# Optimization experiments

Hardware: AMD Instinct MI355X
Metric: run time of the kernel (lower is better)

The kernel has to match this reference:

```python
import jax, jax.numpy as jnp
import numpy as np

WIDTH = 1024
HEADS = 16
INIT_SCALE = 0.02


def setup_inputs() -> dict:
    key = jax.random.key(0)
    ks = jax.random.split(key, 5)
    x = jax.random.normal(ks[0], (2, 2048, WIDTH), dtype=jnp.float32)
    # torch Linear weight [out, in]; we store transposed [in, out] for x @ W
    W_qkv = jax.random.normal(ks[1], (WIDTH, 3 * WIDTH), dtype=jnp.float32) * INIT_SCALE
    b_qkv = jnp.zeros((3 * WIDTH,), dtype=jnp.float32)
    W_proj = jax.random.normal(ks[2], (WIDTH, WIDTH), dtype=jnp.float32) * INIT_SCALE
    b_proj = jnp.zeros((WIDTH,), dtype=jnp.float32)
    return {"x": x, "W_qkv": W_qkv, "b_qkv": b_qkv, "W_proj": W_proj, "b_proj": b_proj}


def reference(x, W_qkv, b_qkv, W_proj, b_proj):
    bs, n_ctx, width = x.shape
    heads = HEADS
    attn_ch = width // heads  # per-head channel dim (width*3 // heads // 3)
    scale = 1.0 / np.sqrt(np.sqrt(attn_ch))  # applied to both q and k

    qkv = x @ W_qkv + b_qkv                      # [b, t, 3*width]
    qkv = qkv.reshape(bs, n_ctx, heads, 3 * attn_ch)
    q, k, v = jnp.split(qkv, 3, axis=-1)         # each [b, t, h, c]

    weight = jnp.einsum('bthc,bshc->bhts', q * scale, k * scale)
    wdtype = weight.dtype
    weight = jax.nn.softmax(weight.astype(jnp.float32), axis=-1).astype(wdtype)

    out = jnp.einsum('bhts,bshc->bthc', weight, v).reshape(bs, n_ctx, width)
    return out @ W_proj + b_proj
```

## Files before the change

### kernel.cpp

```cpp
#include <hip/hip_runtime.h>

typedef __attribute__((ext_vector_type(4))) float fx4;
typedef __attribute__((ext_vector_type(16))) float f32x16;
typedef __attribute__((ext_vector_type(8))) short s16x8;
typedef __attribute__((ext_vector_type(2))) unsigned int u32x2;

#define QK_SCALE 0.35355339059327373f
#define LOG2E    1.4426950408889634f

__device__ __forceinline__ short f2bf(float f) {
  union { float f; unsigned int u; } v; v.f = f;
  unsigned int r = v.u + 0x7fffu + ((v.u >> 16) & 1u);
  return (short)(r >> 16);
}

__device__ __forceinline__ unsigned f2u(float f) {
  union { float f; unsigned u; } v; v.f = f; return v.u;
}
__device__ __forceinline__ float u2f(unsigned u) {
  union { unsigned u; float f; } v; v.u = u; return v.f;
}
__device__ __forceinline__ float bf2f(short s) {
  return u2f(((unsigned)(unsigned short)s) << 16);
}

__device__ __forceinline__ float xhalf_sum(float x) {
  u32x2 r = __builtin_amdgcn_permlane32_swap(f2u(x), f2u(x), false, false);
  return u2f(r[0]) + u2f(r[1]);
}

__device__ __forceinline__ int swz(int row, int cb) {
  return (row * 128 + cb) ^ ((row & 7) << 4);
}

#define GLL(g, lds) __builtin_amdgcn_global_load_lds( \
    (__attribute__((address_space(1))) void*)(void*)(g), \
    (__attribute__((address_space(3))) void*)(void*)(lds), 16, 0, 0)

__global__ __launch_bounds__(256) void prep(
    const float* __restrict__ x, short* __restrict__ x16,
    const float* __restrict__ Wqkv, short* __restrict__ WqkvT,
    const float* __restrict__ Wproj, short* __restrict__ WprojT) {
  const int b = blockIdx.x;
  if (b < 4096) {
    int i = b * 256 + threadIdx.x;
    float4 v = reinterpret_cast<const float4*>(x)[i];
    short4 o;
    o.x = f2bf(v.x); o.y = f2bf(v.y); o.z = f2bf(v.z); o.w = f2bf(v.w);
    reinterpret_cast<short4*>(x16)[i] = o;
    return;
  }
  __shared__ float tile[32][33];
  const float* W; short* WT; int N, bx, by;
  if (b < 7168) { W = Wqkv; WT = WqkvT; N = 3072; int r = b - 4096; bx = r % 96; by = r / 96; }
  else          { W = Wproj; WT = WprojT; N = 1024; int r = b - 7168; bx = r % 32; by = r / 32; }
  const int K = 1024;
  int tx = threadIdx.x & 31, ty = threadIdx.x >> 5;
  int n0 = bx * 32, k0 = by * 32;
#pragma unroll
  for (int i = 0; i < 32; i += 8)
    tile[ty + i][tx] = W[(size_t)(k0 + ty + i) * N + n0 + tx];
  __syncthreads();
#pragma unroll
  for (int i = 0; i < 32; i += 8)
    WT[(size_t)(n0 + ty + i) * K + k0 + tx] = f2bf(tile[tx][ty + i]);
}

template <int MODE, int BK>
__global__ __launch_bounds__(256) void gemm_bf16(
    const short* __restrict__ A, const short* __restrict__ Bt,
    const float* __restrict__ bias, float* __restrict__ Cout,
    short* __restrict__ Qo, short* __restrict__ Ko, short* __restrict__ Vo,
    int M, int N, int K) {
  __shared__ __align__(16) char sA[2][128 * BK * 2];
  __shared__ __align__(16) char sB[2][128 * BK * 2];
  const int tid = threadIdx.x;
  const int w = tid >> 6, l = tid & 63;
  const int lr = l & 15, lg = l >> 4;
  const int bid = blockIdx.x;
  const int m0 = ((bid & 7) * 4 + ((bid >> 3) & 3)) * 128;
  const int n0 = (bid >> 5) * 128;
  const int wr = (w >> 1) * 64, wc = (w & 1) * 64;

  fx4 accT[4][4] = {};

  auto stage = [&](int kt, int buf) {
#pragma unroll
    for (int i = 0; i < (BK == 64 ? 4 : 2); ++i) {
      int c = i * 256 + tid;
      int r, lch;
      if (BK == 64) { r = c >> 3; int p = c & 7; lch = p ^ (r & 7); }
      else          { r = c >> 2; int p = c & 3; lch = p ^ (r & 3); }
      GLL(A + (size_t)(m0 + r) * K + kt + lch * 8, sA[buf] + c * 16);
      GLL(Bt + (size_t)(n0 + r) * K + kt + lch * 8, sB[buf] + c * 16);
    }
  };

  stage(0, 0);
  __syncthreads();

  const int NIT = K / BK;
  int cur = 0;
  for (int it = 0; it < NIT; ++it) {
    if (it + 1 < NIT) stage((it + 1) * BK, cur ^ 1);
#pragma unroll
    for (int kk = 0; kk < (BK == 64 ? 2 : 1); ++kk) {
      s16x8 av[4], bv[4];
#pragma unroll
      for (int m = 0; m < 4; ++m) {
        int R = wr + m * 16 + lr;
        int off = (BK == 64) ? swz(R, kk * 64 + lg * 16)
                             : ((R * 64 + lg * 16) ^ ((R & 3) << 4));
        av[m] = *reinterpret_cast<const s16x8*>(sA[cur] + off);
      }
#pragma unroll
      for (int n = 0; n < 4; ++n) {
        int R = wc + n * 16 + lr;
        int off = (BK == 64) ? swz(R, kk * 64 + lg * 16)
                             : ((R * 64 + lg * 16) ^ ((R & 3) << 4));
        bv[n] = *reinterpret_cast<const s16x8*>(sB[cur] + off);
      }
#pragma unroll
      for (int n = 0; n < 4; ++n)
#pragma unroll
        for (int m = 0; m < 4; ++m)
          accT[n][m] = __builtin_amdgcn_mfma_f32_16x16x32_bf16(bv[n], av[m], accT[n][m], 0, 0, 0);
    }
    __syncthreads();
    cur ^= 1;
  }

#pragma unroll
  for (int n = 0; n < 4; ++n) {
    const int col0 = n0 + wc + n * 16 + lg * 4;
    const float4 bs = *reinterpret_cast<const float4*>(bias + col0);
    if (MODE == 1) {
#pragma unroll
      for (int m = 0; m < 4; ++m) {
        int row = m0 + wr + m * 16 + lr;
        float4 v;
        v.x = accT[n][m][0] + bs.x; v.y = accT[n][m][1] + bs.y;
        v.z = accT[n][m][2] + bs.z; v.w = accT[n][m][3] + bs.w;
        *reinterpret_cast<float4*>(Cout + (size_t)row * N + col0) = v;
      }
    } else {
      const int h = col0 / 192;
      const int rr = col0 - h * 192;
#pragma unroll
      for (int m = 0; m < 4; ++m) {
        int row = m0 + wr + m * 16 + lr;
        int b = row >> 11, t = row & 2047;
        size_t bh = (size_t)b * 16 + h;
        float v0 = accT[n][m][0] + bs.x, v1 = accT[n][m][1] + bs.y;
        float v2 = accT[n][m][2] + bs.z, v3 = accT[n][m][3] + bs.w;
        if (rr < 64) {
          short4 s4;
          s4.x = f2bf(v0 * (QK_SCALE * LOG2E)); s4.y = f2bf(v1 * (QK_SCALE * LOG2E));
          s4.z = f2bf(v2 * (QK_SCALE * LOG2E)); s4.w = f2bf(v3 * (QK_SCALE * LOG2E));
          *reinterpret_cast<short4*>(Qo + (bh * 2048 + t) * 64 + rr) = s4;
        } else if (rr < 128) {
          short4 s4;
          s4.x = f2bf(v0 * QK_SCALE); s4.y = f2bf(v1 * QK_SCALE);
          s4.z = f2bf(v2 * QK_SCALE); s4.w = f2bf(v3 * QK_SCALE);
          *reinterpret_cast<short4*>(Ko + (bh * 2048 + t) * 64 + (rr - 64)) = s4;
        } else {
          Vo[(bh * 64 + (rr - 128) + 0) * 2048 + t] = f2bf(v0);
          Vo[(bh * 64 + (rr - 128) + 1) * 2048 + t] = f2bf(v1);
          Vo[(bh * 64 + (rr - 128) + 2) * 2048 + t] = f2bf(v2);
          Vo[(bh * 64 + (rr - 128) + 3) * 2048 + t] = f2bf(v3);
        }
      }
    }
  }
}

__global__ __launch_bounds__(256, 4) void attn_fwd(
    const short* __restrict__ Q, const short* __restrict__ Kc,
    const short* __restrict__ VT, short* __restrict__ OW,
    float* __restrict__ ML) {
  __shared__ __align__(16) char sK[2][8192];
  __shared__ __align__(16) char sV[2][8192];
  const int tid = threadIdx.x;
  const int w = tid >> 6, l = tid & 63;
  const int l31 = l & 31, hi = l >> 5;
  const int bid = blockIdx.x;
  const int bh = (bid & 7) * 4 + ((bid >> 3) & 3);
  const int rest = bid >> 5;
  const int qt = rest >> 1, half = rest & 1;
  const int q0 = qt * 128 + w * 32;
  const int sbase = half * 1024;

  s16x8 qf[4];
  const short* qp = Q + ((size_t)bh * 2048 + q0 + l31) * 64 + hi * 8;
#pragma unroll
  for (int ks = 0; ks < 4; ++ks)
    qf[ks] = *reinterpret_cast<const s16x8*>(qp + ks * 16);

  float lsum = 0.f;
  f32x16 o0 = {}, o1 = {};

#pragma unroll
  for (int i = 0; i < 2; ++i) {
    int c = i * 256 + tid, r = c >> 3, pch = c & 7, lch = pch ^ (r & 7);
    GLL(Kc + ((size_t)bh * 2048 + sbase + r) * 64 + lch * 8, sK[0] + c * 16);
    GLL(VT + ((size_t)bh * 64 + r) * 2048 + sbase + lch * 8, sV[0] + c * 16);
  }
  __syncthreads();

  for (int sb = 0; sb < 16; ++sb) {
    const int s0 = sbase + sb * 64;
    if (sb < 15) {
#pragma unroll
      for (int i = 0; i < 2; ++i) {
        int c = i * 256 + tid, r = c >> 3, pch = c & 7, lch = pch ^ (r & 7);
        GLL(Kc + ((size_t)bh * 2048 + s0 + 64 + r) * 64 + lch * 8, sK[(sb + 1) & 1] + c * 16);
        GLL(VT + ((size_t)bh * 64 + r) * 2048 + s0 + 64 + lch * 8, sV[(sb + 1) & 1] + c * 16);
      }
    }
    const char* kb = sK[sb & 1];
    const char* vb = sV[sb & 1];

    f32x16 p0 = {}, p1 = {};
    __builtin_amdgcn_s_setprio(1);
#pragma unroll
    for (int ks = 0; ks < 4; ++ks) {
      int off = swz(l31, ks * 32 + hi * 16);
      s16x8 ka0 = *reinterpret_cast<const s16x8*>(kb + off);
      s16x8 ka1 = *reinterpret_cast<const s16x8*>(kb + off + 4096);
      p0 = __builtin_amdgcn_mfma_f32_32x32x16_bf16(ka0, qf[ks], p0, 0, 0, 0);
      p1 = __builtin_amdgcn_mfma_f32_32x32x16_bf16(ka1, qf[ks], p1, 0, 0, 0);
    }
    __builtin_amdgcn_s_setprio(0);

#pragma unroll
    for (int i = 0; i < 16; ++i) {
      p0[i] = __builtin_amdgcn_exp2f(p0[i]);
      p1[i] = __builtin_amdgcn_exp2f(p1[i]);
    }
    float s8[8];
#pragma unroll
    for (int i = 0; i < 8; ++i)
      s8[i] = (p0[2 * i] + p0[2 * i + 1]) + (p1[2 * i] + p1[2 * i + 1]);
    float rs = ((s8[0] + s8[1]) + (s8[2] + s8[3])) + ((s8[4] + s8[5]) + (s8[6] + s8[7]));
    lsum += xhalf_sum(rs);

    int wd[16];
#pragma unroll
    for (int i = 0; i < 8; ++i) {
      asm("v_cvt_pk_bf16_f32 %0, %1, %2" : "=v"(wd[i]) : "v"(p0[2 * i]), "v"(p0[2 * i + 1]));
      asm("v_cvt_pk_bf16_f32 %0, %1, %2" : "=v"(wd[8 + i]) : "v"(p1[2 * i]), "v"(p1[2 * i + 1]));
    }

    __builtin_amdgcn_s_setprio(1);
#pragma unroll
    for (int t = 0; t < 4; ++t) {
      u32x2 s02 = __builtin_amdgcn_permlane32_swap(
          (unsigned)wd[4 * t], (unsigned)wd[4 * t + 2], false, false);
      u32x2 s13 = __builtin_amdgcn_permlane32_swap(
          (unsigned)wd[4 * t + 1], (unsigned)wd[4 * t + 3], false, false);
      union { unsigned i4[4]; s16x8 v; } fr;
      fr.i4[0] = s02[0]; fr.i4[1] = s13[0]; fr.i4[2] = s02[1]; fr.i4[3] = s13[1];
      int off = swz(l31, t * 32 + hi * 16);
      s16x8 v0 = *reinterpret_cast<const s16x8*>(vb + off);
      s16x8 v1 = *reinterpret_cast<const s16x8*>(vb + off + 4096);
      o0 = __builtin_amdgcn_mfma_f32_32x32x16_bf16(v0, fr.v, o0, 0, 0, 0);
      o1 = __builtin_amdgcn_mfma_f32_32x32x16_bf16(v1, fr.v, o1, 0, 0, 0);
    }
    __builtin_amdgcn_s_setprio(0);
    __syncthreads();
  }

  short* owp = OW + (((size_t)(half * 32 + bh) * 2048) + q0 + l31) * 64 + hi * 4;
#pragma unroll
  for (int gq = 0; gq < 4; ++gq) {
    short4 s4;
    s4.x = f2bf(o0[4 * gq]);     s4.y = f2bf(o0[4 * gq + 1]);
    s4.z = f2bf(o0[4 * gq + 2]); s4.w = f2bf(o0[4 * gq + 3]);
    *reinterpret_cast<short4*>(owp + 8 * gq) = s4;
    s4.x = f2bf(o1[4 * gq]);     s4.y = f2bf(o1[4 * gq + 1]);
    s4.z = f2bf(o1[4 * gq + 2]); s4.w = f2bf(o1[4 * gq + 3]);
    *reinterpret_cast<short4*>(owp + 32 + 8 * gq) = s4;
  }
  if (hi == 0)
    ML[(size_t)(half * 32 + bh) * 2048 + q0 + l31] = lsum;
}

__global__ __launch_bounds__(256) void attn_merge(
    const short* __restrict__ OW, const float* __restrict__ ML,
    short* __restrict__ Y) {
  int gid = blockIdx.x * 256 + threadIdx.x;
  int row = gid >> 3, dc = (gid & 7) * 8;
  float inv = 1.f / (ML[row] + ML[65536 + row]);
  s16x8 a = *reinterpret_cast<const s16x8*>(OW + (size_t)row * 64 + dc);
  s16x8 bb = *reinterpret_cast<const s16x8*>(OW + (size_t)65536 * 64 + (size_t)row * 64 + dc);
  int bh = row >> 11, q = row & 2047;
  int b = bh >> 4, h = bh & 15;
  short* yp = Y + ((size_t)b * 2048 + q) * 1024 + h * 64 + dc;
  s16x8 o;
#pragma unroll
  for (int i = 0; i < 8; ++i)
    o[i] = f2bf((bf2f(a[i]) + bf2f(bb[i])) * inv);
  *reinterpret_cast<s16x8*>(yp) = o;
}

extern "C" void kernel_launch(void* const* d_in, const int* in_sizes, int n_in,
                              void* d_out, int out_size, void* d_ws, size_t ws_size,
                              hipStream_t stream) {
  const float* x     = (const float*)d_in[0];
  const float* Wqkv  = (const float*)d_in[1];
  const float* bqkv  = (const float*)d_in[2];
  const float* Wproj = (const float*)d_in[3];
  const float* bproj = (const float*)d_in[4];
  float* out = (float*)d_out;

  char* ws = (char*)d_ws;
  const size_t MB = 1024 * 1024;
  short* x16    = (short*)(ws);
  short* WqkvT  = (short*)(ws + 8 * MB);
  short* WprojT = (short*)(ws + 14 * MB);
  short* Q16    = (short*)(ws + 16 * MB);
  short* K16    = (short*)(ws + 24 * MB);
  short* VT16   = (short*)(ws + 32 * MB);
  short* OW     = (short*)(ws + 40 * MB);
  float* ML     = (float*)(ws + 58 * MB);
  short* Y16    = x16;

  prep<<<8192, 256, 0, stream>>>(x, x16, Wqkv, WqkvT, Wproj, WprojT);
  gemm_bf16<0, 32><<<768, 256, 0, stream>>>(x16, WqkvT, bqkv, nullptr,
                                            Q16, K16, VT16, 4096, 3072, 1024);
  attn_fwd<<<1024, 256, 0, stream>>>(Q16, K16, VT16, OW, ML);
  attn_merge<<<2048, 256, 0, stream>>>(OW, ML, Y16);
  gemm_bf16<1, 64><<<256, 256, 0, stream>>>(Y16, WprojT, bproj, out,
                                            nullptr, nullptr, nullptr, 4096, 1024, 1024);
}
```

Before: 120.5 us.

## Parametrize GEMM tile width, use 8 waves for QKV and narrower proj tiles

The GEMM template gains a BN parameter, and each wave now computes a 64x32 subtile instead of 64x64. The QKV GEMM keeps its 128x128 tiles but runs 512 threads (8 waves) per block. The output projection uses 128x64 tiles, doubling its grid to 512 blocks for better CU coverage. Separately, the attention kernel moves the cross-half row-sum reduction out of the KV loop so it runs once at the end, trading less per-tile shuffle work for more blocks or waves and smaller per-wave reuse.

```diff
diff --git a/kernel.cpp b/kernel.cpp
--- a/kernel.cpp
+++ b/kernel.cpp
@@ -66,34 +66,49 @@
     WT[(size_t)(n0 + ty + i) * K + k0 + tx] = f2bf(tile[tx][ty + i]);
 }
 
-template <int MODE, int BK>
-__global__ __launch_bounds__(256) void gemm_bf16(
+template <int MODE, int BK, int BN>
+__global__ __launch_bounds__(BN * 4, 4) void gemm_bf16(
     const short* __restrict__ A, const short* __restrict__ Bt,
     const float* __restrict__ bias, float* __restrict__ Cout,
     short* __restrict__ Qo, short* __restrict__ Ko, short* __restrict__ Vo,
     int M, int N, int K) {
+  constexpr int T = BN * 4;
+  constexpr int NWC = BN / 32;
+  constexpr int CA = 16 * BK / T;
+  constexpr int CB = BK / 32;
   __shared__ __align__(16) char sA[2][128 * BK * 2];
-  __shared__ __align__(16) char sB[2][128 * BK * 2];
+  __shared__ __align__(16) char sB[2][BN * BK * 2];
   const int tid = threadIdx.x;
   const int w = tid >> 6, l = tid & 63;
   const int lr = l & 15, lg = l >> 4;
   const int bid = blockIdx.x;
   const int m0 = ((bid & 7) * 4 + ((bid >> 3) & 3)) * 128;
-  const int n0 = (bid >> 5) * 128;
-  const int wr = (w >> 1) * 64, wc = (w & 1) * 64;
-
-  fx4 accT[4][4] = {};
+  const int n0 = (bid >> 5) * BN;
+  const int wr = (w / NWC) * 64, wc = (w % NWC) * 32;
+
+  fx4 accT[2][4] = {};
 
   auto stage = [&](int kt, int buf) {
 #pragma unroll
-    for (int i = 0; i < (BK == 64 ? 4 : 2); ++i) {
-      int c = i * 256 + tid;
+    for (int i = 0; i < CA; ++i) {
+      int c = i * T + tid;
       int r, lch;
-      if (BK == 64) { r = c >> 3; int p = c & 7; lch = p ^ (r & 7); }
-      else          { r = c >> 2; int p = c & 3; lch = p ^ (r & 3); }
+      if (BK == 64) { r = c >> 3; lch = (c & 7) ^ (r & 7); }
+      else          { r = c >> 2; lch = (c & 3) ^ (r & 3); }
       GLL(A + (size_t)(m0 + r) * K + kt + lch * 8, sA[buf] + c * 16);
+    }
+#pragma unroll
+    for (int i = 0; i < CB; ++i) {
+      int c = i * T + tid;
+      int r, lch;
+      if (BK == 64) { r = c >> 3; lch = (c & 7) ^ (r & 7); }
+      else          { r = c >> 2; lch = (c & 3) ^ (r & 3); }
       GLL(Bt + (size_t)(n0 + r) * K + kt + lch * 8, sB[buf] + c * 16);
     }
+  };
+  auto roff = [&](int R, int kk) {
+    return (BK == 64) ? ((R * 128 + kk * 64 + lg * 16) ^ ((R & 7) << 4))
+                      : ((R * 64 + lg * 16) ^ ((R & 3) << 4));
   };
 
   stage(0, 0);
@@ -105,23 +120,15 @@
     if (it + 1 < NIT) stage((it + 1) * BK, cur ^ 1);
 #pragma unroll
     for (int kk = 0; kk < (BK == 64 ? 2 : 1); ++kk) {
-      s16x8 av[4], bv[4];
-#pragma unroll
-      for (int m = 0; m < 4; ++m) {
-        int R = wr + m * 16 + lr;
-        int off = (BK == 64) ? swz(R, kk * 64 + lg * 16)
-                             : ((R * 64 + lg * 16) ^ ((R & 3) << 4));
-        av[m] = *reinterpret_cast<const s16x8*>(sA[cur] + off);
-      }
-#pragma unroll
-      for (int n = 0; n < 4; ++n) {
-        int R = wc + n * 16 + lr;
-        int off = (BK == 64) ? swz(R, kk * 64 + lg * 16)
-                             : ((R * 64 + lg * 16) ^ ((R & 3) << 4));
-        bv[n] = *reinterpret_cast<const s16x8*>(sB[cur] + off);
-      }
-#pragma unroll
-      for (int n = 0; n < 4; ++n)
+      s16x8 av[4], bv[2];
+#pragma unroll
+      for (int m = 0; m < 4; ++m)
+        av[m] = *reinterpret_cast<const s16x8*>(sA[cur] + roff(wr + m * 16 + lr, kk));
+#pragma unroll
+      for (int n = 0; n < 2; ++n)
+        bv[n] = *reinterpret_cast<const s16x8*>(sB[cur] + roff(wc + n * 16 + lr, kk));
+#pragma unroll
+      for (int n = 0; n < 2; ++n)
 #pragma unroll
         for (int m = 0; m < 4; ++m)
           accT[n][m] = __builtin_amdgcn_mfma_f32_16x16x32_bf16(bv[n], av[m], accT[n][m], 0, 0, 0);
@@ -131,7 +138,7 @@
   }
 
 #pragma unroll
-  for (int n = 0; n < 4; ++n) {
+  for (int n = 0; n < 2; ++n) {
     const int col0 = n0 + wc + n * 16 + lg * 4;
     const float4 bs = *reinterpret_cast<const float4*>(bias + col0);
     if (MODE == 1) {
@@ -241,8 +248,7 @@
 #pragma unroll
     for (int i = 0; i < 8; ++i)
       s8[i] = (p0[2 * i] + p0[2 * i + 1]) + (p1[2 * i] + p1[2 * i + 1]);
-    float rs = ((s8[0] + s8[1]) + (s8[2] + s8[3])) + ((s8[4] + s8[5]) + (s8[6] + s8[7]));
-    lsum += xhalf_sum(rs);
+    lsum += ((s8[0] + s8[1]) + (s8[2] + s8[3])) + ((s8[4] + s8[5]) + (s8[6] + s8[7]));
 
     int wd[16];
 #pragma unroll
@@ -281,8 +287,9 @@
     s4.z = f2bf(o1[4 * gq + 2]); s4.w = f2bf(o1[4 * gq + 3]);
     *reinterpret_cast<short4*>(owp + 32 + 8 * gq) = s4;
   }
+  float lt = xhalf_sum(lsum);
   if (hi == 0)
-    ML[(size_t)(half * 32 + bh) * 2048 + q0 + l31] = lsum;
+    ML[(size_t)(half * 32 + bh) * 2048 + q0 + l31] = lt;
 }
 
 __global__ __launch_bounds__(256) void attn_merge(
@@ -326,10 +333,10 @@
   short* Y16    = x16;
 
   prep<<<8192, 256, 0, stream>>>(x, x16, Wqkv, WqkvT, Wproj, WprojT);
-  gemm_bf16<0, 32><<<768, 256, 0, stream>>>(x16, WqkvT, bqkv, nullptr,
-                                            Q16, K16, VT16, 4096, 3072, 1024);
+  gemm_bf16<0, 32, 128><<<768, 512, 0, stream>>>(x16, WqkvT, bqkv, nullptr,
+                                                 Q16, K16, VT16, 4096, 3072, 1024);
   attn_fwd<<<1024, 256, 0, stream>>>(Q16, K16, VT16, OW, ML);
   attn_merge<<<2048, 256, 0, stream>>>(OW, ML, Y16);
-  gemm_bf16<1, 64><<<256, 256, 0, stream>>>(Y16, WprojT, bproj, out,
-                                            nullptr, nullptr, nullptr, 4096, 1024, 1024);
-}
+  gemm_bf16<1, 64, 64><<<512, 256, 0, stream>>>(Y16, WprojT, bproj, out,
+                                                nullptr, nullptr, nullptr, 4096, 1024, 1024);
+}
```

After: 116.8 us. -3.1%, faster.
